# Kernel optimization log

Measured on AMD Instinct MI355X. Metric: run time of the kernel, lower is better.

## Reference

```python
import jax, jax.numpy as jnp
import numpy as np

B, LC, LE, D, M = 128, 256, 1024, 256, 512
NEG = -1e9


def setup_inputs() -> dict:
    key = jax.random.key(0)
    ks = jax.random.split(key, 10)
    s = 0.02
    return {
        "criteria": jax.random.normal(ks[0], (B, LC, D), jnp.float32),
        "ehr": jax.random.normal(ks[1], (B, LE, D), jnp.float32),
        "criteria_mask": jax.random.randint(ks[2], (B, LC), 0, 2, jnp.int32),
        "ehr_mask": jax.random.randint(ks[3], (B, LE), 0, 2, jnp.int32),
        # params stored (in, out); torch Linear is x @ W.T + b
        "Wa": jax.random.normal(ks[4], (D, D), jnp.float32) * s,
        "ba": jnp.zeros((D,), jnp.float32),
        "Wr": jax.random.normal(ks[5], (2 * D, D), jnp.float32) * s,
        "br": jnp.zeros((D,), jnp.float32),
        "Wm": jax.random.normal(ks[6], (4 * D, M), jnp.float32) * s,
        "bm": jnp.zeros((M,), jnp.float32),
        "Wo": jax.random.normal(ks[7], (M, 3), jnp.float32) * s,
        "bo": jnp.zeros((3,), jnp.float32),
    }


def reference(criteria, ehr, Wa, ba, Wr, br, Wm, bm, Wo, bo,
              criteria_mask, ehr_mask):
    relu = jax.nn.relu
    c = relu(criteria @ Wa + ba)              # (B, Lc, D)
    e = relu(ehr @ Wa + ba)                   # (B, Le, D)
    align = jnp.einsum("bld,bed->ble", c, e)  # (B, Lc, Le)

    cm = criteria_mask.astype(align.dtype)
    em = ehr_mask.astype(align.dtype)
    # beta: softmax over Lc (dim=1), masked by criteria_mask along Lc
    beta = jax.nn.softmax(align + (1.0 - cm)[:, :, None] * NEG, axis=1)
    # alpha: softmax over Le (dim=1 of transposed), masked by ehr_mask along Le
    alpha = jax.nn.softmax(align + (1.0 - em)[:, None, :] * NEG, axis=2)

    # (alpha.unsqueeze(-1) * ehr.unsqueeze(1)).sum(2) == alpha @ ehr
    att_c = jnp.einsum("ble,bed->bld", alpha, ehr)        # (B, Lc, D)
    r1 = relu(jnp.concatenate([att_c, criteria], axis=-1) @ Wr + br).sum(axis=1)  # (B, D)

    # (beta.unsqueeze(-1) * criteria.unsqueeze(2)).sum(1) == beta.T @ criteria
    att_e = jnp.einsum("ble,bld->bed", beta, criteria)    # (B, Le, D)
    r2 = relu(jnp.concatenate([att_e, ehr], axis=-1) @ Wr + br).sum(axis=1)       # (B, D)

    m = jnp.concatenate([r1, r2, r1 * r2, r1 - r2], axis=-1)  # (B, 4D)
    return relu(m @ Wm + bm) @ Wo + bo                        # (B, 3)
```

## Files before the change

kernel.cpp:

```cpp
#include <hip/hip_runtime.h>
#include <hip/hip_bf16.h>

#define BB 128
#define LC 256
#define LE 1024
#define DD 256
#define MM 512

typedef short bf16x8 __attribute__((ext_vector_type(8)));
typedef unsigned short u16x8 __attribute__((ext_vector_type(8)));
typedef unsigned short u16x4 __attribute__((ext_vector_type(4)));
typedef float f32x4 __attribute__((ext_vector_type(4)));

__device__ __forceinline__ unsigned short f2bfu(float f) {
  unsigned int x = __float_as_uint(f);
  return (unsigned short)((x + 0x7fffu + ((x >> 16) & 1u)) >> 16);
}

__device__ __forceinline__ int lx(int r, int q) {
  return r * 32 + (((q ^ ((r >> 1) & 3)) & 3) << 3);
}

__device__ __forceinline__ void gll16(const unsigned short* g, unsigned short* l) {
  __builtin_amdgcn_global_load_lds((const __attribute__((address_space(1))) void*)g,
                                   (__attribute__((address_space(3))) void*)l, 16, 0, 0);
}

__device__ __forceinline__ void stg128(unsigned short* S, const unsigned short* g,
                                       long ldu, int tid) {
  const int l = tid & 63, w = tid >> 6;
  const int r = w * 16 + (l >> 2), q = l & 3;
  gll16(g + (long)r * ldu + (((q ^ ((r >> 1) & 3)) & 3) << 3), S + w * 512);
}

__device__ __forceinline__ void stg256(unsigned short* S, const unsigned short* g,
                                       long ldu, int tid) {
  const int l = tid & 63, w = tid >> 6;
#pragma unroll
  for (int it = 0; it < 2; ++it) {
    const int r = it * 128 + w * 16 + (l >> 2), q = l & 3;
    gll16(g + (long)r * ldu + (((q ^ ((r >> 1) & 3)) & 3) << 3), S + it * 4096 + w * 512);
  }
}

__device__ __forceinline__ void stg128_256(unsigned short* S, const unsigned short* g,
                                           long ldu, int tid) {
  const int l = tid & 63, w = tid >> 6;
#pragma unroll
  for (int it = 0; it < 2; ++it) {
    const int r = it * 64 + w * 16 + (l >> 2), q = l & 3;
    gll16(g + (long)r * ldu + (((q ^ ((r >> 1) & 3)) & 3) << 3), S + it * 2048 + w * 512);
  }
}

__device__ __forceinline__ void mma_step(const unsigned short* As, const unsigned short* Bs,
                                         f32x4 (&acc)[4][4], int wm, int wn, int lane) {
  const int lm = lane & 15, quad = lane >> 4;
  bf16x8 a[4], b[4];
#pragma unroll
  for (int i = 0; i < 4; ++i) {
    a[i] = *(const bf16x8*)&As[lx(wm * 64 + i * 16 + lm, quad)];
    b[i] = *(const bf16x8*)&Bs[lx(wn * 64 + i * 16 + lm, quad)];
  }
  __builtin_amdgcn_s_setprio(1);
#pragma unroll
  for (int i = 0; i < 4; ++i)
#pragma unroll
    for (int j = 0; j < 4; ++j)
      acc[i][j] = __builtin_amdgcn_mfma_f32_16x16x32_bf16(a[i], b[j], acc[i][j], 0, 0, 0);
  __builtin_amdgcn_s_setprio(0);
}

template <int MT, int NT>
__device__ __forceinline__ void mma_tiles(const unsigned short* As, const unsigned short* Bs,
                                          f32x4 (&acc)[MT][NT], int m0, int n0, int lane) {
  const int lm = lane & 15, quad = lane >> 4;
  bf16x8 a[MT], b[NT];
#pragma unroll
  for (int i = 0; i < MT; ++i)
    a[i] = *(const bf16x8*)&As[lx(m0 + i * 16 + lm, quad)];
#pragma unroll
  for (int j = 0; j < NT; ++j)
    b[j] = *(const bf16x8*)&Bs[lx(n0 + j * 16 + lm, quad)];
  __builtin_amdgcn_s_setprio(1);
#pragma unroll
  for (int i = 0; i < MT; ++i)
#pragma unroll
    for (int j = 0; j < NT; ++j)
      acc[i][j] = __builtin_amdgcn_mfma_f32_16x16x32_bf16(a[i], b[j], acc[i][j], 0, 0, 0);
  __builtin_amdgcn_s_setprio(0);
}

__global__ void zero_kernel(float* __restrict__ p, int n) {
  int i = blockIdx.x * 256 + threadIdx.x;
  if (i < n) p[i] = 0.f;
}

__global__ void wconv_kernel(const float* __restrict__ Wa, const float* __restrict__ Wr,
                             unsigned short* __restrict__ WaT, unsigned short* __restrict__ WrT) {
  int i = blockIdx.x * 256 + threadIdx.x;
  if (i < 65536) WaT[i] = f2bfu(Wa[(i & 255) * 256 + (i >> 8)]);
  if (i < 131072) WrT[i] = f2bfu(Wr[(long)(i & 511) * 256 + (i >> 9)]);
}

__global__ void transT_kernel(const float* __restrict__ src, const int* __restrict__ mask,
                              unsigned short* __restrict__ dstT, unsigned short* __restrict__ dstN,
                              int R, int C) {
  __shared__ unsigned short T2[64 * 258];
  const int tid = threadIdx.x, b = blockIdx.z;
  const int r0 = blockIdx.y * 256, c0 = blockIdx.x * 64;
  const float* s = src + (long)b * R * C;
  const int* mk = mask + (long)b * R;
  unsigned short* dT = dstT + (long)b * R * C;
  unsigned short* dN = dstN + (long)b * R * C;
  const int c4 = tid & 15, rb = tid >> 4;
#pragma unroll
  for (int i = 0; i < 16; ++i) {
    int r = rb + i * 16;
    float4 v = *(const float4*)(s + (long)(r0 + r) * C + c0 + c4 * 4);
    u16x4 nat;
    nat[0] = f2bfu(v.x); nat[1] = f2bfu(v.y); nat[2] = f2bfu(v.z); nat[3] = f2bfu(v.w);
    *(u16x4*)(dN + (long)(r0 + r) * C + c0 + c4 * 4) = nat;
    float g = mk[r0 + r] ? 1.f : 0.f;
    T2[(c4 * 4 + 0) * 258 + r] = f2bfu(v.x * g);
    T2[(c4 * 4 + 1) * 258 + r] = f2bfu(v.y * g);
    T2[(c4 * 4 + 2) * 258 + r] = f2bfu(v.z * g);
    T2[(c4 * 4 + 3) * 258 + r] = f2bfu(v.w * g);
  }
  __syncthreads();
  const int dlo = tid >> 4, rs = (tid & 15) * 8;
#pragma unroll
  for (int dd = 0; dd < 4; ++dd) {
    const int d = dlo + dd * 16;
#pragma unroll
    for (int j = 0; j < 2; ++j) {
      const int r = rs + j * 128;
      *(u16x8*)(dT + (long)(c0 + d) * R + r0 + r) = *(const u16x8*)&T2[d * 258 + r];
    }
  }
}

__global__ __launch_bounds__(256, 2) void proj_mfma(const unsigned short* __restrict__ AN,
                                                    const unsigned short* __restrict__ WaT,
                                                    const float* __restrict__ ba,
                                                    unsigned short* __restrict__ out) {
  __shared__ unsigned short SL[3 * 8192];
  const int tid = threadIdx.x, lane = tid & 63, w = tid >> 6, wm = w >> 1, wn = w & 1;
  const long m0 = (long)blockIdx.y * 128;
  const int n0 = blockIdx.x * 128;
  f32x4 acc[4][4] = {};
  stg128_256(SL, AN + m0 * DD, DD, tid);
  stg128_256(SL + 4096, WaT + (long)n0 * DD, DD, tid);
  stg128_256(SL + 8192, AN + m0 * DD + 32, DD, tid);
  stg128_256(SL + 8192 + 4096, WaT + (long)n0 * DD + 32, DD, tid);
#pragma unroll
  for (int s = 0; s < 8; ++s) {
    if (s == 7) asm volatile("s_waitcnt vmcnt(0) lgkmcnt(0)" ::: "memory");
    else        asm volatile("s_waitcnt vmcnt(4) lgkmcnt(0)" ::: "memory");
    __builtin_amdgcn_s_barrier();
    if (s < 6) {
      unsigned short* d = SL + ((s + 2) % 3) * 8192;
      stg128_256(d, AN + m0 * DD + (s + 2) * 32, DD, tid);
      stg128_256(d + 4096, WaT + (long)n0 * DD + (s + 2) * 32, DD, tid);
    }
    const unsigned short* base = SL + (s % 3) * 8192;
    mma_step(base, base + 4096, acc, wm, wn, lane);
  }
  const int lm = lane & 15, quad = lane >> 4;
#pragma unroll
  for (int i = 0; i < 4; ++i)
#pragma unroll
    for (int j = 0; j < 4; ++j) {
      int col = n0 + wn * 64 + j * 16 + lm;
      float bias = ba[col];
#pragma unroll
      for (int r = 0; r < 4; ++r) {
        long row = m0 + wm * 64 + i * 16 + quad * 4 + r;
        float v = acc[i][j][r] + bias;
        out[row * DD + col] = f2bfu(v > 0.f ? v : 0.f);
      }
    }
}

template <int NCH>
__device__ __forceinline__ void attn_body(
    unsigned short* SLOT, unsigned short* S4,
    const unsigned short* resB, const unsigned short* aSrc,
    const unsigned short* pvB, long pvLd,
    const int* mask, unsigned short* outp, int tid) {
  const int lane = tid & 63, w = tid >> 6;
  const int lm = lane & 15, quad = lane >> 4;
  const int wmS = w >> 2, wnS = w & 3;
  const int wm = w >> 2, wn = w & 3;
  float* asum_s = (float*)SLOT;
  f32x4 acc[4][4] = {};
  float ap0 = 0.f, ap1 = 0.f;
  stg128(SLOT, aSrc, DD, tid);
  stg128(SLOT + 4096, resB, DD, tid);
  stg128(SLOT + 8192, aSrc + 32, DD, tid);
  stg128(SLOT + 8192 + 4096, resB + 32, DD, tid);
  for (int ch = 0; ch < NCH; ++ch) {
    const unsigned short* Ag = aSrc + (long)ch * 128 * DD;
    const unsigned short* Pg = pvB + (long)ch * 128;
    f32x4 accS[4][2] = {};
#pragma unroll
    for (int s = 0; s < 8; ++s) {
      asm volatile("s_waitcnt vmcnt(2) lgkmcnt(0)" ::: "memory");
      __builtin_amdgcn_s_barrier();
      if (s < 6) {
        unsigned short* d = SLOT + ((s + 2) % 3) * 8192;
        stg128(d, Ag + (s + 2) * 32, DD, tid);
        stg128(d + 4096, resB + (s + 2) * 32, DD, tid);
      } else if (s == 6) {
        stg256(SLOT + 2 * 8192, Pg, pvLd, tid);
      } else {
        stg256(SLOT, Pg + 32, pvLd, tid);
      }
      const unsigned short* base = SLOT + (s % 3) * 8192;
      mma_tiles<4, 2>(base, base + 4096, accS, wmS * 64, wnS * 32, lane);
    }
#pragma unroll
    for (int i = 0; i < 4; ++i) {
      const int A0 = wmS * 64 + i * 16 + quad * 4;
      const int4 m4 = *(const int4*)(mask + ch * 128 + A0);
      const float g0 = m4.x ? 1.f : 0.f, g1 = m4.y ? 1.f : 0.f;
      const float g2 = m4.z ? 1.f : 0.f, g3 = m4.w ? 1.f : 0.f;
      const int kk = A0 >> 5, wi = A0 & 31;
      const int qq = wi >> 3, sub = wi & 7;
#pragma unroll
      for (int j = 0; j < 2; ++j) {
        const int row = wnS * 32 + j * 16 + lm;
        float e0 = __expf(accS[i][j][0]);
        float e1 = __expf(accS[i][j][1]);
        float e2 = __expf(accS[i][j][2]);
        float e3 = __expf(accS[i][j][3]);
        float sm = g0 * e0 + g1 * e1 + g2 * e2 + g3 * e3;
        if (j == 0) ap0 += sm; else ap1 += sm;
        u16x4 pk;
        pk[0] = f2bfu(e0); pk[1] = f2bfu(e1); pk[2] = f2bfu(e2); pk[3] = f2bfu(e3);
        *(u16x4*)&S4[kk * 4096 + row * 32 + ((qq ^ ((row >> 1) & 3)) << 3) + sub] = pk;
      }
    }
#pragma unroll
    for (int kk = 0; kk < 4; ++kk) {
      if ((kk == 3) && (ch == NCH - 1))
        asm volatile("s_waitcnt vmcnt(0) lgkmcnt(0)" ::: "memory");
      else
        asm volatile("s_waitcnt vmcnt(2) lgkmcnt(0)" ::: "memory");
      __builtin_amdgcn_s_barrier();
      if (kk < 2) {
        stg256(SLOT + ((kk + 1) % 3) * 8192, Pg + (kk + 2) * 32, pvLd, tid);
      } else if (ch + 1 < NCH) {
        unsigned short* d = SLOT + (kk - 2) * 8192;
        stg128(d, aSrc + (long)(ch + 1) * 128 * DD + (kk - 2) * 32, DD, tid);
        stg128(d + 4096, resB + (kk - 2) * 32, DD, tid);
      }
      mma_tiles<4, 4>(S4 + kk * 4096, SLOT + ((kk + 2) % 3) * 8192, acc,
                      wm * 64, wn * 64, lane);
    }
  }
  if (tid < 128) asum_s[tid] = 0.f;
  __syncthreads();
  {
    float s = ap0;
    s += __shfl_xor(s, 16); s += __shfl_xor(s, 32);
    if (quad == 0) atomicAdd(&asum_s[wnS * 32 + lm], s);
    float t = ap1;
    t += __shfl_xor(t, 16); t += __shfl_xor(t, 32);
    if (quad == 0) atomicAdd(&asum_s[wnS * 32 + 16 + lm], t);
  }
  __syncthreads();
  float rs[4][4];
#pragma unroll
  for (int i = 0; i < 4; ++i)
#pragma unroll
    for (int r = 0; r < 4; ++r)
      rs[i][r] = 1.f / asum_s[wm * 64 + i * 16 + quad * 4 + r];
#pragma unroll
  for (int i = 0; i < 4; ++i)
#pragma unroll
    for (int j = 0; j < 4; ++j) {
      int col = wn * 64 + j * 16 + lm;
#pragma unroll
      for (int r = 0; r < 4; ++r) {
        int row = wm * 64 + i * 16 + quad * 4 + r;
        outp[(long)row * DD + col] = f2bfu(acc[i][j][r] * rs[i][r]);
      }
    }
}

__global__ __launch_bounds__(512, 2) void attn_fused(
    const unsigned short* __restrict__ cB, const unsigned short* __restrict__ eB,
    const unsigned short* __restrict__ ehrTm, const unsigned short* __restrict__ critTm,
    const int* __restrict__ em, const int* __restrict__ cm,
    unsigned short* __restrict__ attc, unsigned short* __restrict__ atte) {
  __shared__ unsigned short SLOT[3 * 8192];
  __shared__ unsigned short S4[16384];
  const int tid = threadIdx.x, fid = blockIdx.x;
  if (fid < 256) {
    const int lid = (fid & 7) * 32 + (fid >> 3);
    const int b = lid >> 1, m0 = (lid & 1) * 128;
    attn_body<8>(SLOT, S4, cB + ((long)b * LC + m0) * DD, eB + (long)b * LE * DD,
                 ehrTm + (long)b * DD * LE, LE, em + (long)b * LE,
                 attc + ((long)b * LC + m0) * DD, tid);
  } else {
    const int f = fid - 256;
    const int lid = (f & 7) * 128 + (f >> 3);
    const int b = lid >> 3, n0 = (lid & 7) * 128;
    attn_body<2>(SLOT, S4, eB + ((long)b * LE + n0) * DD, cB + (long)b * LC * DD,
                 critTm + (long)b * DD * LC, LC, cm + (long)b * LC,
                 atte + ((long)b * LE + n0) * DD, tid);
  }
}

__global__ __launch_bounds__(256, 2) void rsum_mfma(const unsigned short* __restrict__ att,
                                                    const unsigned short* __restrict__ origB,
                                                    const unsigned short* __restrict__ WrT,
                                                    const float* __restrict__ br,
                                                    float* __restrict__ rout, int Lseq) {
  __shared__ unsigned short SL[3 * 8192];
  __shared__ float red[2][128];
  const int tid = threadIdx.x, lane = tid & 63, w = tid >> 6, wm = w >> 1, wn = w & 1;
  const long m0 = (long)blockIdx.y * 128;
  const int n0 = blockIdx.x * 128;
  const int b = (int)(m0 / Lseq);
  f32x4 acc[4][4] = {};
  stg128_256(SL, att + m0 * DD, DD, tid);
  stg128_256(SL + 4096, WrT + (long)n0 * 512, 512, tid);
  stg128_256(SL + 8192, att + m0 * DD + 32, DD, tid);
  stg128_256(SL + 8192 + 4096, WrT + (long)n0 * 512 + 32, 512, tid);
#pragma unroll
  for (int s = 0; s < 16; ++s) {
    if (s == 15) asm volatile("s_waitcnt vmcnt(0) lgkmcnt(0)" ::: "memory");
    else         asm volatile("s_waitcnt vmcnt(4) lgkmcnt(0)" ::: "memory");
    __builtin_amdgcn_s_barrier();
    if (s < 14) {
      const int k1 = (s + 2) * 32;
      const unsigned short* aS =
          (k1 < DD) ? att + m0 * DD + k1 : origB + m0 * DD + (k1 - DD);
      unsigned short* d = SL + ((s + 2) % 3) * 8192;
      stg128_256(d, aS, DD, tid);
      stg128_256(d + 4096, WrT + (long)n0 * 512 + k1, 512, tid);
    }
    const unsigned short* base = SL + (s % 3) * 8192;
    mma_step(base, base + 4096, acc, wm, wn, lane);
  }
  const int lm = lane & 15, quad = lane >> 4;
#pragma unroll
  for (int j = 0; j < 4; ++j) {
    int col = n0 + wn * 64 + j * 16 + lm;
    float bias = br[col];
    float s = 0.f;
#pragma unroll
    for (int i = 0; i < 4; ++i)
#pragma unroll
      for (int r = 0; r < 4; ++r) {
        float v = acc[i][j][r] + bias;
        s += v > 0.f ? v : 0.f;
      }
    s += __shfl_xor(s, 16);
    s += __shfl_xor(s, 32);
    if (quad == 0) red[wm][wn * 64 + j * 16 + lm] = s;
  }
  __syncthreads();
  if (tid < 128)
    atomicAdd(&rout[b * DD + n0 + tid], red[0][tid] + red[1][tid]);
}

__global__ void mbuild_kernel(const float* __restrict__ r1, const float* __restrict__ r2,
                              unsigned short* __restrict__ mB) {
  int i = blockIdx.x * 256 + threadIdx.x;
  int b = i >> 8, d = i & 255;
  float v1 = r1[i], v2 = r2[i];
  unsigned short* row = mB + (long)b * 1024;
  row[d] = f2bfu(v1);
  row[256 + d] = f2bfu(v2);
  row[512 + d] = f2bfu(v1 * v2);
  row[768 + d] = f2bfu(v1 - v2);
}

__global__ __launch_bounds__(256, 2) void mlp_mfma(const unsigned short* __restrict__ mB,
                                                   const float* __restrict__ Wm,
                                                   float* __restrict__ h) {
  __shared__ unsigned short As[4096], Bs[4096];
  const int tid = threadIdx.x, lane = tid & 63, w = tid >> 6, wm = w >> 1, wn = w & 1;
  const int n0 = blockIdx.x * 128;
  const int kb = blockIdx.y * 256;
  f32x4 acc[4][4] = {};
  for (int k0 = kb; k0 < kb + 256; k0 += 32) {
    stg128_256(As, mB + k0, 1024, tid);
    {
      const int dcc = tid & 7, er = tid >> 3;
#pragma unroll
      for (int i = 0; i < 4; ++i) {
        int nch = dcc + i * 8;
        float4 v = *(const float4*)(Wm + (long)(k0 + er) * MM + n0 + nch * 4);
        float vv[4] = {v.x, v.y, v.z, v.w};
#pragma unroll
        for (int q = 0; q < 4; ++q)
          Bs[lx(nch * 4 + q, er >> 3) + (er & 7)] = f2bfu(vv[q]);
      }
    }
    __syncthreads();
    mma_step(As, Bs, acc, wm, wn, lane);
    __syncthreads();
  }
  const int lm = lane & 15, quad = lane >> 4;
#pragma unroll
  for (int i = 0; i < 4; ++i)
#pragma unroll
    for (int j = 0; j < 4; ++j) {
      int col = n0 + wn * 64 + j * 16 + lm;
#pragma unroll
      for (int r = 0; r < 4; ++r) {
        int row = wm * 64 + i * 16 + quad * 4 + r;
        atomicAdd(&h[(long)row * MM + col], acc[i][j][r]);
      }
    }
}

__global__ void out3_kernel(const float* __restrict__ h, const float* __restrict__ Wo,
                            const float* __restrict__ bm, const float* __restrict__ bo,
                            float* __restrict__ out) {
  const int b = blockIdx.x, tid = threadIdx.x, lane = tid & 63, w = tid >> 6;
  __shared__ float red[4][3];
  float a[3] = {0.f, 0.f, 0.f};
  for (int k = tid; k < MM; k += 256) {
    float hv = h[(long)b * MM + k] + bm[k];
    hv = hv > 0.f ? hv : 0.f;
    a[0] += hv * Wo[k * 3 + 0];
    a[1] += hv * Wo[k * 3 + 1];
    a[2] += hv * Wo[k * 3 + 2];
  }
#pragma unroll
  for (int o = 0; o < 3; ++o) {
    a[o] += __shfl_xor(a[o], 1);  a[o] += __shfl_xor(a[o], 2);
    a[o] += __shfl_xor(a[o], 4);  a[o] += __shfl_xor(a[o], 8);
    a[o] += __shfl_xor(a[o], 16); a[o] += __shfl_xor(a[o], 32);
    if (lane == 0) red[w][o] = a[o];
  }
  __syncthreads();
  if (tid < 3)
    out[b * 3 + tid] = red[0][tid] + red[1][tid] + red[2][tid] + red[3][tid] + bo[tid];
}

extern "C" void kernel_launch(void* const* d_in, const int* in_sizes, int n_in,
                              void* d_out, int out_size, void* d_ws, size_t ws_size,
                              hipStream_t stream) {
  const float* criteria = (const float*)d_in[0];
  const float* ehr      = (const float*)d_in[1];
  const int*   cmask    = (const int*)d_in[2];
  const int*   emask    = (const int*)d_in[3];
  const float* Wa       = (const float*)d_in[4];
  const float* ba       = (const float*)d_in[5];
  const float* Wr       = (const float*)d_in[6];
  const float* br       = (const float*)d_in[7];
  const float* Wm       = (const float*)d_in[8];
  const float* bm       = (const float*)d_in[9];
  const float* Wo       = (const float*)d_in[10];
  const float* bo       = (const float*)d_in[11];
  float* out = (float*)d_out;

  char* ws = (char*)d_ws;
  unsigned short* cB     = (unsigned short*)(ws);
  unsigned short* eB     = (unsigned short*)(ws + 16777216);
  unsigned short* ehrTm  = (unsigned short*)(ws + 83886080);
  unsigned short* critTm = (unsigned short*)(ws + 150994944);
  unsigned short* ehrN   = (unsigned short*)(ws + 167772160);
  unsigned short* critN  = (unsigned short*)(ws + 234881024);
  unsigned short* attc   = (unsigned short*)(ws + 251658240);
  unsigned short* atteP  = (unsigned short*)(ws + 268435456);
  float* r1   = (float*)(ws + 335544320);
  float* r2   = (float*)(ws + 335675392);
  float* hbuf = (float*)(ws + 335806464);
  unsigned short* WaT = (unsigned short*)(ws + 336068608);
  unsigned short* WrT = (unsigned short*)(ws + 336199680);
  unsigned short* mB  = (unsigned short*)(ws + 336461824);

  dim3 blk(256);
  zero_kernel<<<dim3(512), blk, 0, stream>>>(r1, 131072);
  wconv_kernel<<<dim3(512), blk, 0, stream>>>(Wa, Wr, WaT, WrT);
  transT_kernel<<<dim3(DD / 64, LE / 256, BB), blk, 0, stream>>>(ehr, emask, ehrTm, ehrN, LE, DD);
  transT_kernel<<<dim3(DD / 64, LC / 256, BB), blk, 0, stream>>>(criteria, cmask, critTm, critN, LC, DD);
  proj_mfma<<<dim3(2, (BB * LC) / 128), blk, 0, stream>>>(critN, WaT, ba, cB);
  proj_mfma<<<dim3(2, (BB * LE) / 128), blk, 0, stream>>>(ehrN, WaT, ba, eB);
  attn_fused<<<dim3(1280), dim3(512), 0, stream>>>(cB, eB, ehrTm, critTm, emask, cmask,
                                                   attc, atteP);
  rsum_mfma<<<dim3(2, (BB * LC) / 128), blk, 0, stream>>>(attc, critN, WrT, br, r1, LC);
  rsum_mfma<<<dim3(2, (BB * LE) / 128), blk, 0, stream>>>(atteP, ehrN, WrT, br, r2, LE);
  mbuild_kernel<<<dim3(BB), blk, 0, stream>>>(r1, r2, mB);
  mlp_mfma<<<dim3(MM / 128, 4), blk, 0, stream>>>(mB, Wm, hbuf);
  out3_kernel<<<dim3(BB), blk, 0, stream>>>(hbuf, Wo, bm, bo, out);
}
```

Baseline: 530.8 us.

## Deepen attention LDS staging ring from three to six slots

```diff
diff --git a/kernel.cpp b/kernel.cpp
--- a/kernel.cpp
+++ b/kernel.cpp
@@ -195,28 +195,33 @@
   float* asum_s = (float*)SLOT;
   f32x4 acc[4][4] = {};
   float ap0 = 0.f, ap1 = 0.f;
-  stg128(SLOT, aSrc, DD, tid);
-  stg128(SLOT + 4096, resB, DD, tid);
-  stg128(SLOT + 8192, aSrc + 32, DD, tid);
-  stg128(SLOT + 8192 + 4096, resB + 32, DD, tid);
+#pragma unroll
+  for (int i = 0; i < 5; ++i) {
+    stg128(SLOT + i * 8192, aSrc + i * 32, DD, tid);
+    stg128(SLOT + i * 8192 + 4096, resB + i * 32, DD, tid);
+  }
   for (int ch = 0; ch < NCH; ++ch) {
     const unsigned short* Ag = aSrc + (long)ch * 128 * DD;
+    const unsigned short* An = aSrc + (long)(ch + 1) * 128 * DD;
     const unsigned short* Pg = pvB + (long)ch * 128;
+    const bool last = (ch == NCH - 1);
     f32x4 accS[4][2] = {};
 #pragma unroll
     for (int s = 0; s < 8; ++s) {
-      asm volatile("s_waitcnt vmcnt(2) lgkmcnt(0)" ::: "memory");
+      asm volatile("s_waitcnt vmcnt(8) lgkmcnt(0)" ::: "memory");
       __builtin_amdgcn_s_barrier();
-      if (s < 6) {
-        unsigned short* d = SLOT + ((s + 2) % 3) * 8192;
-        stg128(d, Ag + (s + 2) * 32, DD, tid);
-        stg128(d + 4096, resB + (s + 2) * 32, DD, tid);
-      } else if (s == 6) {
-        stg256(SLOT + 2 * 8192, Pg, pvLd, tid);
-      } else {
-        stg256(SLOT, Pg + 32, pvLd, tid);
-      }
-      const unsigned short* base = SLOT + (s % 3) * 8192;
+      if (s < 3) {
+        unsigned short* d = SLOT + ((s + 5) % 6) * 8192;
+        stg128(d, Ag + (s + 5) * 32, DD, tid);
+        stg128(d + 4096, resB + (s + 5) * 32, DD, tid);
+      } else if (s < 7) {
+        stg256(SLOT + ((s + 5) % 6) * 8192, Pg + (s - 3) * 32, pvLd, tid);
+      } else if (!last) {
+        unsigned short* d = SLOT + ((s + 5) % 6) * 8192;
+        stg128(d, An, DD, tid);
+        stg128(d + 4096, resB, DD, tid);
+      }
+      const unsigned short* base = SLOT + (s % 6) * 8192;
       mma_tiles<4, 2>(base, base + 4096, accS, wmS * 64, wnS * 32, lane);
     }
 #pragma unroll
@@ -243,19 +248,21 @@
     }
 #pragma unroll
     for (int kk = 0; kk < 4; ++kk) {
-      if ((kk == 3) && (ch == NCH - 1))
-        asm volatile("s_waitcnt vmcnt(0) lgkmcnt(0)" ::: "memory");
-      else
-        asm volatile("s_waitcnt vmcnt(2) lgkmcnt(0)" ::: "memory");
+      if (last) {
+        if (kk == 0)      asm volatile("s_waitcnt vmcnt(6) lgkmcnt(0)" ::: "memory");
+        else if (kk == 1) asm volatile("s_waitcnt vmcnt(4) lgkmcnt(0)" ::: "memory");
+        else if (kk == 2) asm volatile("s_waitcnt vmcnt(2) lgkmcnt(0)" ::: "memory");
+        else              asm volatile("s_waitcnt vmcnt(0) lgkmcnt(0)" ::: "memory");
+      } else {
+        asm volatile("s_waitcnt vmcnt(8) lgkmcnt(0)" ::: "memory");
+      }
       __builtin_amdgcn_s_barrier();
-      if (kk < 2) {
-        stg256(SLOT + ((kk + 1) % 3) * 8192, Pg + (kk + 2) * 32, pvLd, tid);
-      } else if (ch + 1 < NCH) {
-        unsigned short* d = SLOT + (kk - 2) * 8192;
-        stg128(d, aSrc + (long)(ch + 1) * 128 * DD + (kk - 2) * 32, DD, tid);
-        stg128(d + 4096, resB + (kk - 2) * 32, DD, tid);
-      }
-      mma_tiles<4, 4>(S4 + kk * 4096, SLOT + ((kk + 2) % 3) * 8192, acc,
+      if (!last) {
+        unsigned short* d = SLOT + ((kk + 13) % 6) * 8192;
+        stg128(d, An + (kk + 1) * 32, DD, tid);
+        stg128(d + 4096, resB + (kk + 1) * 32, DD, tid);
+      }
+      mma_tiles<4, 4>(S4 + kk * 4096, SLOT + ((kk + 8) % 6) * 8192, acc,
                       wm * 64, wn * 64, lane);
     }
   }
@@ -294,7 +301,7 @@
     const unsigned short* __restrict__ ehrTm, const unsigned short* __restrict__ critTm,
     const int* __restrict__ em, const int* __restrict__ cm,
     unsigned short* __restrict__ attc, unsigned short* __restrict__ atte) {
-  __shared__ unsigned short SLOT[3 * 8192];
+  __shared__ unsigned short SLOT[6 * 8192];
   __shared__ unsigned short S4[16384];
   const int tid = threadIdx.x, fid = blockIdx.x;
   if (fid < 256) {
```

New measurement: 521.8 us. Within noise of the previous version (-1.7%).
